# Optimization experiments

Measured on AMD Instinct MI355X. Metric: run time of the kernel, lower is better.

Reference implementation:

```python
import jax, jax.numpy as jnp
import numpy as np

EPS = 1e-5  # InstanceNorm2d default eps


def setup_inputs() -> dict:
    key = jax.random.key(0)
    ks = jax.random.split(key, 5)
    B, T, C, N, H = 4, 8, 256, 196, 4
    s = 1.0 / np.sqrt(C)
    return {
        "emb": jax.random.normal(ks[0], (B, T, C, N), dtype=jnp.float32),
        "Wq": jax.random.normal(ks[1], (H, C, C), dtype=jnp.float32) * s,
        "Wk": jax.random.normal(ks[2], (H, C, C), dtype=jnp.float32) * s,
        "Wv": jax.random.normal(ks[3], (H, C, C), dtype=jnp.float32) * s,
        "Wo": jax.random.normal(ks[4], (C, C), dtype=jnp.float32) * s,
    }


def reference(emb, Wq, Wk, Wv, Wo):
    B, T, C, N = emb.shape
    S = T * N  # KV_size
    # emb.permute(0,1,3,2).view(B, T*N, C)
    x = jnp.transpose(emb, (0, 1, 3, 2)).reshape(B, S, C)
    # per-head full-width Linear projections (nn.Linear: y = x @ W.T)
    Q = jnp.einsum("bsc,hdc->bhsd", x, Wq)  # [B,H,S,C]
    K = jnp.einsum("bsc,hdc->bhsd", x, Wk)
    V = jnp.einsum("bsc,hdc->bhsd", x, Wv)
    scores = jnp.einsum("bhsd,bhtd->bhst", Q, K) / jnp.sqrt(jnp.float32(S))
    # InstanceNorm2d over each [S,S] map per (batch, head), no affine, biased var
    mean = jnp.mean(scores, axis=(-2, -1), keepdims=True)
    var = jnp.var(scores, axis=(-2, -1), keepdims=True)
    normed = (scores - mean) * jax.lax.rsqrt(var + EPS)
    probs = jax.nn.softmax(normed, axis=-1)  # attn_dropout: eval-mode identity
    ctx = jnp.einsum("bhst,bhtd->bhsd", probs, V)  # [B,H,S,C]
    ctx = jnp.mean(ctx, axis=1)  # mean over heads -> [B,S,C]
    O1 = jnp.einsum("bsc,dc->bsd", ctx, Wo)  # out Linear; proj_dropout identity
    # .view(-1, num_frames, num_channels, num_patches) on contiguous [B, T*N, C]
    return O1.reshape(B, T, C, N)
```

## Files before the change

kernel.cpp:

```cpp
#include <hip/hip_runtime.h>
#include <stdint.h>

typedef unsigned short u16;

#define Bb 4
#define Hh 4
#define Tt 8
#define Cc 256
#define NP 196
#define Ss 1568
#define SCALE_S 0.0252538136f

typedef __attribute__((ext_vector_type(4))) float floatx4;
typedef __attribute__((ext_vector_type(8))) short shortx8;

__device__ __forceinline__ float bf2f(u16 u) {
    union { unsigned u; float f; } v; v.u = ((unsigned)u) << 16; return v.f;
}
__device__ __forceinline__ u16 f2bf(float f) {
    union { float f; unsigned u; } v; v.f = f;
    unsigned r = v.u + 0x7FFFu + ((v.u >> 16) & 1u);
    return (u16)(r >> 16);
}

__global__ __launch_bounds__(256) void k_convw(const float* __restrict__ src, u16* __restrict__ dst, int n) {
    int i = blockIdx.x * 256 + threadIdx.x;
    if (i < n) dst[i] = f2bf(src[i]);
}

__device__ __forceinline__ void mfma_step(const u16* As, const u16* Bs, int lane,
                                          int wm, int wn, floatx4 acc[4][4]) {
    const int r15 = lane & 15;
    const int kq  = (lane >> 4) << 3;
    shortx8 a[4], b[4];
#pragma unroll
    for (int i = 0; i < 4; ++i)
        a[i] = *(const shortx8*)(As + (wm * 64 + i * 16 + r15) * 32 + kq);
#pragma unroll
    for (int j = 0; j < 4; ++j)
        b[j] = *(const shortx8*)(Bs + (wn * 64 + j * 16 + r15) * 32 + kq);
#pragma unroll
    for (int i = 0; i < 4; ++i)
#pragma unroll
        for (int j = 0; j < 4; ++j)
            acc[i][j] = __builtin_amdgcn_mfma_f32_16x16x32_bf16(a[i], b[j], acc[i][j], 0, 0, 0);
}

__device__ __forceinline__ void gemm_bt_core(const u16* A, const u16* Bm, int lda, int ldb,
                                             int mbase, int mlast, int nbase, int nlast,
                                             int KD, u16* As, u16* Bs, floatx4 acc[4][4]) {
    int tid = threadIdx.x;
    int lane = tid & 63, wave = tid >> 6, wm = wave >> 1, wn = wave & 1;
    int row0 = tid >> 2, row1 = 64 + (tid >> 2);
    int cole = (tid & 3) << 3;
    int ga0 = mbase + row0; ga0 = ga0 <= mlast ? ga0 : mlast;
    int ga1 = mbase + row1; ga1 = ga1 <= mlast ? ga1 : mlast;
    int gb0 = nbase + row0; gb0 = gb0 <= nlast ? gb0 : nlast;
    int gb1 = nbase + row1; gb1 = gb1 <= nlast ? gb1 : nlast;
    const u16* pa0 = A  + (size_t)ga0 * lda + cole;
    const u16* pa1 = A  + (size_t)ga1 * lda + cole;
    const u16* pb0 = Bm + (size_t)gb0 * ldb + cole;
    const u16* pb1 = Bm + (size_t)gb1 * ldb + cole;
    shortx8 va0 = *(const shortx8*)(pa0);
    shortx8 va1 = *(const shortx8*)(pa1);
    shortx8 vb0 = *(const shortx8*)(pb0);
    shortx8 vb1 = *(const shortx8*)(pb1);
    for (int k0 = 0; k0 < KD; k0 += 32) {
        __syncthreads();
        *(shortx8*)(As + row0 * 32 + cole) = va0;
        *(shortx8*)(As + row1 * 32 + cole) = va1;
        *(shortx8*)(Bs + row0 * 32 + cole) = vb0;
        *(shortx8*)(Bs + row1 * 32 + cole) = vb1;
        int k1 = k0 + 32;
        if (k1 < KD) {
            va0 = *(const shortx8*)(pa0 + k1);
            va1 = *(const shortx8*)(pa1 + k1);
            vb0 = *(const shortx8*)(pb0 + k1);
            vb1 = *(const shortx8*)(pb1 + k1);
        }
        __syncthreads();
        mfma_step(As, Bs, lane, wm, wn, acc);
    }
}

__global__ void k_transpose(const float* __restrict__ emb, u16* __restrict__ x) {
    __shared__ u16 tile[32][33];
    int bt = blockIdx.z;
    int c0 = blockIdx.y * 32, n0 = blockIdx.x * 32;
    const float* src = emb + (size_t)bt * Cc * NP;
#pragma unroll
    for (int rr = 0; rr < 32; rr += 8) {
        int c = c0 + threadIdx.y + rr;
        int n = n0 + threadIdx.x;
        u16 v = 0;
        if (n < NP) v = f2bf(src[(size_t)c * NP + n]);
        tile[threadIdx.y + rr][threadIdx.x] = v;
    }
    __syncthreads();
    int b = bt / Tt, t = bt % Tt;
    u16* dst = x + ((size_t)b * Ss + (size_t)t * NP) * Cc;
#pragma unroll
    for (int rr = 0; rr < 32; rr += 8) {
        int n = n0 + threadIdx.y + rr;
        int c = c0 + threadIdx.x;
        if (n < NP) dst[(size_t)n * Cc + c] = tile[threadIdx.x][threadIdx.y + rr];
    }
}

__global__ __launch_bounds__(256) void k_qkv(const u16* __restrict__ x,
                                             const u16* __restrict__ Wq,
                                             const u16* __restrict__ Wk,
                                             const u16* __restrict__ Wv,
                                             u16* __restrict__ Q, u16* __restrict__ Kb,
                                             u16* __restrict__ Vt) {
    __shared__ __align__(16) u16 As[128 * 32], Bs[128 * 32];
    floatx4 acc[4][4];
#pragma unroll
    for (int i = 0; i < 4; ++i)
#pragma unroll
        for (int j = 0; j < 4; ++j) acc[i][j] = (floatx4)(0.f);
    int z = blockIdx.z;
    int qkv = z >> 4, bh = z & 15, b = bh >> 2, h = bh & 3;
    const u16* A = x + (size_t)b * Ss * Cc;
    const u16* W = (qkv == 0 ? Wq : (qkv == 1 ? Wk : Wv)) + (size_t)h * Cc * Cc;
    int mbase = blockIdx.y * 128, nbase = blockIdx.x * 128;
    gemm_bt_core(A, W, Cc, Cc, mbase, Ss - 1, nbase, Cc - 1, Cc, As, Bs, acc);

    int tid = threadIdx.x, lane = tid & 63, wave = tid >> 6, wm = wave >> 1, wn = wave & 1;
    int rq = (lane >> 4) << 2, cn = lane & 15;
    if (qkv < 2) {
        u16* out = (qkv == 0 ? Q : Kb) + (size_t)bh * Ss * Cc;
#pragma unroll
        for (int i = 0; i < 4; ++i) {
            int mb = mbase + wm * 64 + i * 16 + rq;
#pragma unroll
            for (int j = 0; j < 4; ++j) {
                int n = nbase + wn * 64 + j * 16 + cn;
#pragma unroll
                for (int r = 0; r < 4; ++r) {
                    int m = mb + r;
                    if (m < Ss) out[(size_t)m * Cc + n] = f2bf(acc[i][j][r]);
                }
            }
        }
    } else {
        u16* out = Vt + (size_t)bh * Cc * Ss;
#pragma unroll
        for (int i = 0; i < 4; ++i) {
            int m0 = mbase + wm * 64 + i * 16 + rq;
            if (m0 < Ss) {
#pragma unroll
                for (int j = 0; j < 4; ++j) {
                    int n = nbase + wn * 64 + j * 16 + cn;
                    ushort4 v;
                    v.x = f2bf(acc[i][j][0]); v.y = f2bf(acc[i][j][1]);
                    v.z = f2bf(acc[i][j][2]); v.w = f2bf(acc[i][j][3]);
                    *(ushort4*)(out + (size_t)n * Ss + m0) = v;
                }
            }
        }
    }
}

__global__ __launch_bounds__(256) void k_scores(const u16* __restrict__ Q,
                                                const u16* __restrict__ Kb,
                                                u16* __restrict__ Sc, float* __restrict__ stats) {
    __shared__ __align__(16) u16 As[128 * 32], Bs[128 * 32];
    __shared__ float sred[8];
    floatx4 acc[4][4];
#pragma unroll
    for (int i = 0; i < 4; ++i)
#pragma unroll
        for (int j = 0; j < 4; ++j) acc[i][j] = (floatx4)(0.f);
    int bh = blockIdx.z;
    const u16* A  = Q  + (size_t)bh * Ss * Cc;
    const u16* Bm = Kb + (size_t)bh * Ss * Cc;
    int mbase = blockIdx.y * 128, nbase = blockIdx.x * 128;
    gemm_bt_core(A, Bm, Cc, Cc, mbase, Ss - 1, nbase, Ss - 1, Cc, As, Bs, acc);

    int tid = threadIdx.x, lane = tid & 63, wave = tid >> 6, wm = wave >> 1, wn = wave & 1;
    int rq = (lane >> 4) << 2, cn = lane & 15;
    u16* out = Sc + (size_t)bh * Ss * Ss;
    float lsum = 0.f, lsq = 0.f;
#pragma unroll
    for (int i = 0; i < 4; ++i) {
        int mb = mbase + wm * 64 + i * 16 + rq;
#pragma unroll
        for (int j = 0; j < 4; ++j) {
            int n = nbase + wn * 64 + j * 16 + cn;
            bool nv = n < Ss;
#pragma unroll
            for (int r = 0; r < 4; ++r) {
                int m = mb + r;
                if (nv && m < Ss) {
                    float v = acc[i][j][r] * SCALE_S;
                    out[(size_t)m * Ss + n] = f2bf(v);
                    lsum += v; lsq += v * v;
                }
            }
        }
    }
#pragma unroll
    for (int mk = 1; mk <= 32; mk <<= 1) { lsum += __shfl_xor(lsum, mk); lsq += __shfl_xor(lsq, mk); }
    if (lane == 0) { sred[wave] = lsum; sred[4 + wave] = lsq; }
    __syncthreads();
    if (tid == 0) atomicAdd(&stats[bh * 4 + 0], sred[0] + sred[1] + sred[2] + sred[3]);
    if (tid == 1) atomicAdd(&stats[bh * 4 + 1], sred[4] + sred[5] + sred[6] + sred[7]);
}

__global__ void k_stats(float* __restrict__ stats) {
    int i = threadIdx.x;
    if (i < 16) {
        float inv  = 1.f / ((float)Ss * (float)Ss);
        float mean = stats[i * 4] * inv;
        float var  = stats[i * 4 + 1] * inv - mean * mean;
        var = fmaxf(var, 0.f);
        stats[i * 4 + 2] = mean;
        stats[i * 4 + 3] = rsqrtf(var + 1e-5f);
    }
}

__global__ __launch_bounds__(256) void k_pv(const u16* __restrict__ Sc,
                                            const u16* __restrict__ Vt,
                                            const float* __restrict__ stats,
                                            float* __restrict__ ctxm) {
    __shared__ __align__(16) u16 As[128 * 32], Bs[128 * 32];
    __shared__ float rs[128];
    floatx4 acc[4][4];
#pragma unroll
    for (int i = 0; i < 4; ++i)
#pragma unroll
        for (int j = 0; j < 4; ++j) acc[i][j] = (floatx4)(0.f);
    int bh = blockIdx.z;
    float mean = stats[bh * 4 + 2], istd = stats[bh * 4 + 3];
    float aa = istd * 1.44269504f;
    float bb = -mean * aa;
    const u16* A  = Sc + (size_t)bh * Ss * Ss;
    const u16* Bm = Vt + (size_t)bh * Cc * Ss;
    int mbase = blockIdx.y * 128, nbase = blockIdx.x * 128;
    int tid = threadIdx.x, lane = tid & 63, wave = tid >> 6, wm = wave >> 1, wn = wave & 1;
    int row0 = tid >> 2, row1 = 64 + (tid >> 2);
    int cole = (tid & 3) << 3;
    int ga0 = mbase + row0; ga0 = ga0 <= Ss - 1 ? ga0 : Ss - 1;
    int ga1 = mbase + row1; ga1 = ga1 <= Ss - 1 ? ga1 : Ss - 1;
    const u16* pa0 = A + (size_t)ga0 * Ss + cole;
    const u16* pa1 = A + (size_t)ga1 * Ss + cole;
    const u16* pb0 = Bm + (size_t)(nbase + row0) * Ss + cole;
    const u16* pb1 = Bm + (size_t)(nbase + row1) * Ss + cole;
    float rsum0 = 0.f, rsum1 = 0.f;
    shortx8 v0 = *(const shortx8*)(pa0);
    shortx8 v1 = *(const shortx8*)(pa1);
    shortx8 vb0 = *(const shortx8*)(pb0);
    shortx8 vb1 = *(const shortx8*)(pb1);

    for (int k0 = 0; k0 < Ss; k0 += 32) {
        shortx8 o0, o1;
        float p0 = 0.f, p1 = 0.f;
#pragma unroll
        for (int e = 0; e < 8; ++e) {
            float f0 = bf2f((u16)v0[e]);
            float e0 = exp2f(f0 * aa + bb);
            p0 += e0; o0[e] = (short)f2bf(e0);
            float f1 = bf2f((u16)v1[e]);
            float e1 = exp2f(f1 * aa + bb);
            p1 += e1; o1[e] = (short)f2bf(e1);
        }
        rsum0 += p0; rsum1 += p1;
        __syncthreads();
        *(shortx8*)(As + row0 * 32 + cole) = o0;
        *(shortx8*)(As + row1 * 32 + cole) = o1;
        *(shortx8*)(Bs + row0 * 32 + cole) = vb0;
        *(shortx8*)(Bs + row1 * 32 + cole) = vb1;
        int k1 = k0 + 32;
        if (k1 < Ss) {
            v0  = *(const shortx8*)(pa0 + k1);
            v1  = *(const shortx8*)(pa1 + k1);
            vb0 = *(const shortx8*)(pb0 + k1);
            vb1 = *(const shortx8*)(pb1 + k1);
        }
        __syncthreads();
        mfma_step(As, Bs, lane, wm, wn, acc);
    }
    rsum0 += __shfl_xor(rsum0, 1); rsum0 += __shfl_xor(rsum0, 2);
    rsum1 += __shfl_xor(rsum1, 1); rsum1 += __shfl_xor(rsum1, 2);
    __syncthreads();
    if ((tid & 3) == 0) { rs[tid >> 2] = rsum0; rs[64 + (tid >> 2)] = rsum1; }
    __syncthreads();

    int b = bh >> 2;
    float* outp = ctxm + (size_t)b * Ss * Cc;
    int rq = (lane >> 4) << 2, cn = lane & 15;
#pragma unroll
    for (int i = 0; i < 4; ++i) {
        int ml = wm * 64 + i * 16 + rq;
#pragma unroll
        for (int r = 0; r < 4; ++r) {
            int m = mbase + ml + r;
            if (m < Ss) {
                float invs = 0.25f / rs[ml + r];
#pragma unroll
                for (int j = 0; j < 4; ++j) {
                    int n = nbase + wn * 64 + j * 16 + cn;
                    atomicAdd(&outp[(size_t)m * Cc + n], acc[i][j][r] * invs);
                }
            }
        }
    }
}

__global__ __launch_bounds__(256) void k_out(const float* __restrict__ ctxm,
                                             const u16* __restrict__ Wo, float* __restrict__ out) {
    __shared__ __align__(16) u16 As[128 * 32], Bs[128 * 32];
    floatx4 acc[4][4];
#pragma unroll
    for (int i = 0; i < 4; ++i)
#pragma unroll
        for (int j = 0; j < 4; ++j) acc[i][j] = (floatx4)(0.f);
    int b = blockIdx.z;
    const float* A = ctxm + (size_t)b * Ss * Cc;
    int mbase = blockIdx.y * 128, nbase = blockIdx.x * 128;
    int tid = threadIdx.x, lane = tid & 63, wave = tid >> 6, wm = wave >> 1, wn = wave & 1;
    int row0 = tid >> 2, row1 = 64 + (tid >> 2);
    int cole = (tid & 3) << 3;
    int ga0 = mbase + row0; ga0 = ga0 <= Ss - 1 ? ga0 : Ss - 1;
    int ga1 = mbase + row1; ga1 = ga1 <= Ss - 1 ? ga1 : Ss - 1;
    const float* pa0 = A + (size_t)ga0 * Cc + cole;
    const float* pa1 = A + (size_t)ga1 * Cc + cole;
    const u16* pb0 = Wo + (size_t)(nbase + row0 <= Cc - 1 ? nbase + row0 : Cc - 1) * Cc + cole;
    const u16* pb1 = Wo + (size_t)(nbase + row1 <= Cc - 1 ? nbase + row1 : Cc - 1) * Cc + cole;
    float4 a00 = *(const float4*)(pa0), a01 = *(const float4*)(pa0 + 4);
    float4 a10 = *(const float4*)(pa1), a11 = *(const float4*)(pa1 + 4);
    shortx8 vb0 = *(const shortx8*)(pb0);
    shortx8 vb1 = *(const shortx8*)(pb1);
    for (int k0 = 0; k0 < Cc; k0 += 32) {
        shortx8 o0, o1;
        o0[0] = (short)f2bf(a00.x); o0[1] = (short)f2bf(a00.y); o0[2] = (short)f2bf(a00.z); o0[3] = (short)f2bf(a00.w);
        o0[4] = (short)f2bf(a01.x); o0[5] = (short)f2bf(a01.y); o0[6] = (short)f2bf(a01.z); o0[7] = (short)f2bf(a01.w);
        o1[0] = (short)f2bf(a10.x); o1[1] = (short)f2bf(a10.y); o1[2] = (short)f2bf(a10.z); o1[3] = (short)f2bf(a10.w);
        o1[4] = (short)f2bf(a11.x); o1[5] = (short)f2bf(a11.y); o1[6] = (short)f2bf(a11.z); o1[7] = (short)f2bf(a11.w);
        __syncthreads();
        *(shortx8*)(As + row0 * 32 + cole) = o0;
        *(shortx8*)(As + row1 * 32 + cole) = o1;
        *(shortx8*)(Bs + row0 * 32 + cole) = vb0;
        *(shortx8*)(Bs + row1 * 32 + cole) = vb1;
        int k1 = k0 + 32;
        if (k1 < Cc) {
            a00 = *(const float4*)(pa0 + k1); a01 = *(const float4*)(pa0 + k1 + 4);
            a10 = *(const float4*)(pa1 + k1); a11 = *(const float4*)(pa1 + k1 + 4);
            vb0 = *(const shortx8*)(pb0 + k1);
            vb1 = *(const shortx8*)(pb1 + k1);
        }
        __syncthreads();
        mfma_step(As, Bs, lane, wm, wn, acc);
    }
    int rq = (lane >> 4) << 2, cn = lane & 15;
    float* o = out + (size_t)b * Ss * Cc;
#pragma unroll
    for (int i = 0; i < 4; ++i) {
        int mb = mbase + wm * 64 + i * 16 + rq;
#pragma unroll
        for (int j = 0; j < 4; ++j) {
            int n = nbase + wn * 64 + j * 16 + cn;
#pragma unroll
            for (int r = 0; r < 4; ++r) {
                int m = mb + r;
                if (m < Ss) o[(size_t)m * Cc + n] = acc[i][j][r];
            }
        }
    }
}

extern "C" void kernel_launch(void* const* d_in, const int* in_sizes, int n_in,
                              void* d_out, int out_size, void* d_ws, size_t ws_size,
                              hipStream_t stream) {
    const float* emb = (const float*)d_in[0];
    float* out = (float*)d_out;

    char* ws = (char*)d_ws;
    size_t off = 0;
    auto alloc = [&](size_t bytes) -> void* {
        void* p = ws + off;
        off = (off + bytes + 255) & ~(size_t)255;
        return p;
    };
    float* stats = (float*)alloc(16 * 4 * sizeof(float));
    u16* Wqc  = (u16*)alloc((size_t)Hh * Cc * Cc * 2);
    u16* Wkc  = (u16*)alloc((size_t)Hh * Cc * Cc * 2);
    u16* Wvc  = (u16*)alloc((size_t)Hh * Cc * Cc * 2);
    u16* Woc  = (u16*)alloc((size_t)Cc * Cc * 2);
    u16* x    = (u16*)alloc((size_t)Bb * Ss * Cc * 2);
    u16* Q    = (u16*)alloc((size_t)Bb * Hh * Ss * Cc * 2);
    u16* Kb   = (u16*)alloc((size_t)Bb * Hh * Ss * Cc * 2);
    u16* Vt   = (u16*)alloc((size_t)Bb * Hh * Ss * Cc * 2);
    float* ctxm = (float*)alloc((size_t)Bb * Ss * Cc * 4);
    u16* Sc   = (u16*)alloc((size_t)Bb * Hh * Ss * Ss * 2);

    hipMemsetAsync(stats, 0, 16 * 4 * sizeof(float), stream);
    hipMemsetAsync(ctxm, 0, (size_t)Bb * Ss * Cc * 4, stream);

    k_convw<<<dim3(1024), dim3(256), 0, stream>>>((const float*)d_in[1], Wqc, Hh * Cc * Cc);
    k_convw<<<dim3(1024), dim3(256), 0, stream>>>((const float*)d_in[2], Wkc, Hh * Cc * Cc);
    k_convw<<<dim3(1024), dim3(256), 0, stream>>>((const float*)d_in[3], Wvc, Hh * Cc * Cc);
    k_convw<<<dim3(256),  dim3(256), 0, stream>>>((const float*)d_in[4], Woc, Cc * Cc);

    k_transpose<<<dim3(7, 8, 32), dim3(32, 8), 0, stream>>>(emb, x);
    k_qkv<<<dim3(2, 13, 48), dim3(256), 0, stream>>>(x, Wqc, Wkc, Wvc, Q, Kb, Vt);
    k_scores<<<dim3(13, 13, 16), dim3(256), 0, stream>>>(Q, Kb, Sc, stats);
    k_stats<<<dim3(1), dim3(64), 0, stream>>>(stats);
    k_pv<<<dim3(2, 13, 16), dim3(256), 0, stream>>>(Sc, Vt, stats, ctxm);
    k_out<<<dim3(2, 13, 4), dim3(256), 0, stream>>>(ctxm, Woc, out);
}
```

Baseline: 255.1 us.

## Pad LDS rows, double-depth register prefetch, merge weight-convert and stats kernels

Shared-memory tiles get a padded row stride of 40 elements to reduce LDS bank conflicts on the MFMA fragment reads. The GEMM core and k_pv now keep two K-slices of global loads in flight in registers, giving more latency hiding at the cost of extra registers. The four weight-conversion launches are merged into one kernel writing a single contiguous buffer. The tiny k_stats kernel is removed, with the mean and istd computed inline in k_pv, cutting launch overhead.

```diff
diff --git a/kernel.cpp b/kernel.cpp
--- a/kernel.cpp
+++ b/kernel.cpp
@@ -10,6 +10,7 @@
 #define NP 196
 #define Ss 1568
 #define SCALE_S 0.0252538136f
+#define LST 40
 
 typedef __attribute__((ext_vector_type(4))) float floatx4;
 typedef __attribute__((ext_vector_type(8))) short shortx8;
@@ -23,9 +24,20 @@
     return (u16)(r >> 16);
 }
 
-__global__ __launch_bounds__(256) void k_convw(const float* __restrict__ src, u16* __restrict__ dst, int n) {
+__global__ __launch_bounds__(256) void k_convall(const float* __restrict__ Wq,
+                                                 const float* __restrict__ Wk,
+                                                 const float* __restrict__ Wv,
+                                                 const float* __restrict__ Wo,
+                                                 u16* __restrict__ dst) {
+    const int NW = Hh * Cc * Cc;
     int i = blockIdx.x * 256 + threadIdx.x;
-    if (i < n) dst[i] = f2bf(src[i]);
+    float v;
+    if (i < NW) v = Wq[i];
+    else if (i < 2 * NW) v = Wk[i - NW];
+    else if (i < 3 * NW) v = Wv[i - 2 * NW];
+    else if (i < 3 * NW + Cc * Cc) v = Wo[i - 3 * NW];
+    else return;
+    dst[i] = f2bf(v);
 }
 
 __device__ __forceinline__ void mfma_step(const u16* As, const u16* Bs, int lane,
@@ -35,10 +47,10 @@
     shortx8 a[4], b[4];
 #pragma unroll
     for (int i = 0; i < 4; ++i)
-        a[i] = *(const shortx8*)(As + (wm * 64 + i * 16 + r15) * 32 + kq);
+        a[i] = *(const shortx8*)(As + (wm * 64 + i * 16 + r15) * LST + kq);
 #pragma unroll
     for (int j = 0; j < 4; ++j)
-        b[j] = *(const shortx8*)(Bs + (wn * 64 + j * 16 + r15) * 32 + kq);
+        b[j] = *(const shortx8*)(Bs + (wn * 64 + j * 16 + r15) * LST + kq);
 #pragma unroll
     for (int i = 0; i < 4; ++i)
 #pragma unroll
@@ -51,7 +63,7 @@
                                              int KD, u16* As, u16* Bs, floatx4 acc[4][4]) {
     int tid = threadIdx.x;
     int lane = tid & 63, wave = tid >> 6, wm = wave >> 1, wn = wave & 1;
-    int row0 = tid >> 2, row1 = 64 + (tid >> 2);
+    int row0 = tid >> 2, row1 = 64 + row0;
     int cole = (tid & 3) << 3;
     int ga0 = mbase + row0; ga0 = ga0 <= mlast ? ga0 : mlast;
     int ga1 = mbase + row1; ga1 = ga1 <= mlast ? ga1 : mlast;
@@ -61,25 +73,37 @@
     const u16* pa1 = A  + (size_t)ga1 * lda + cole;
     const u16* pb0 = Bm + (size_t)gb0 * ldb + cole;
     const u16* pb1 = Bm + (size_t)gb1 * ldb + cole;
-    shortx8 va0 = *(const shortx8*)(pa0);
-    shortx8 va1 = *(const shortx8*)(pa1);
-    shortx8 vb0 = *(const shortx8*)(pb0);
-    shortx8 vb1 = *(const shortx8*)(pb1);
-    for (int k0 = 0; k0 < KD; k0 += 32) {
-        __syncthreads();
-        *(shortx8*)(As + row0 * 32 + cole) = va0;
-        *(shortx8*)(As + row1 * 32 + cole) = va1;
-        *(shortx8*)(Bs + row0 * 32 + cole) = vb0;
-        *(shortx8*)(Bs + row1 * 32 + cole) = vb1;
-        int k1 = k0 + 32;
-        if (k1 < KD) {
-            va0 = *(const shortx8*)(pa0 + k1);
-            va1 = *(const shortx8*)(pa1 + k1);
-            vb0 = *(const shortx8*)(pb0 + k1);
-            vb1 = *(const shortx8*)(pb1 + k1);
+    shortx8 xa0 = *(const shortx8*)(pa0),      xa1 = *(const shortx8*)(pa1);
+    shortx8 xb0 = *(const shortx8*)(pb0),      xb1 = *(const shortx8*)(pb1);
+    shortx8 ya0 = *(const shortx8*)(pa0 + 32), ya1 = *(const shortx8*)(pa1 + 32);
+    shortx8 yb0 = *(const shortx8*)(pb0 + 32), yb1 = *(const shortx8*)(pb1 + 32);
+    for (int k0 = 0; k0 < KD; k0 += 64) {
+        __syncthreads();
+        *(shortx8*)(As + row0 * LST + cole) = xa0;
+        *(shortx8*)(As + row1 * LST + cole) = xa1;
+        *(shortx8*)(Bs + row0 * LST + cole) = xb0;
+        *(shortx8*)(Bs + row1 * LST + cole) = xb1;
+        int kp = k0 + 64;
+        if (kp < KD) {
+            xa0 = *(const shortx8*)(pa0 + kp); xa1 = *(const shortx8*)(pa1 + kp);
+            xb0 = *(const shortx8*)(pb0 + kp); xb1 = *(const shortx8*)(pb1 + kp);
         }
         __syncthreads();
         mfma_step(As, Bs, lane, wm, wn, acc);
+        if (k0 + 32 < KD) {
+            __syncthreads();
+            *(shortx8*)(As + row0 * LST + cole) = ya0;
+            *(shortx8*)(As + row1 * LST + cole) = ya1;
+            *(shortx8*)(Bs + row0 * LST + cole) = yb0;
+            *(shortx8*)(Bs + row1 * LST + cole) = yb1;
+            int kq2 = k0 + 96;
+            if (kq2 < KD) {
+                ya0 = *(const shortx8*)(pa0 + kq2); ya1 = *(const shortx8*)(pa1 + kq2);
+                yb0 = *(const shortx8*)(pb0 + kq2); yb1 = *(const shortx8*)(pb1 + kq2);
+            }
+            __syncthreads();
+            mfma_step(As, Bs, lane, wm, wn, acc);
+        }
     }
 }
 
@@ -108,12 +132,10 @@
 }
 
 __global__ __launch_bounds__(256) void k_qkv(const u16* __restrict__ x,
-                                             const u16* __restrict__ Wq,
-                                             const u16* __restrict__ Wk,
-                                             const u16* __restrict__ Wv,
+                                             const u16* __restrict__ Wall,
                                              u16* __restrict__ Q, u16* __restrict__ Kb,
                                              u16* __restrict__ Vt) {
-    __shared__ __align__(16) u16 As[128 * 32], Bs[128 * 32];
+    __shared__ __align__(16) u16 As[128 * LST], Bs[128 * LST];
     floatx4 acc[4][4];
 #pragma unroll
     for (int i = 0; i < 4; ++i)
@@ -122,7 +144,7 @@
     int z = blockIdx.z;
     int qkv = z >> 4, bh = z & 15, b = bh >> 2, h = bh & 3;
     const u16* A = x + (size_t)b * Ss * Cc;
-    const u16* W = (qkv == 0 ? Wq : (qkv == 1 ? Wk : Wv)) + (size_t)h * Cc * Cc;
+    const u16* W = Wall + (size_t)qkv * Hh * Cc * Cc + (size_t)h * Cc * Cc;
     int mbase = blockIdx.y * 128, nbase = blockIdx.x * 128;
     gemm_bt_core(A, W, Cc, Cc, mbase, Ss - 1, nbase, Cc - 1, Cc, As, Bs, acc);
 
@@ -165,7 +187,7 @@
 __global__ __launch_bounds__(256) void k_scores(const u16* __restrict__ Q,
                                                 const u16* __restrict__ Kb,
                                                 u16* __restrict__ Sc, float* __restrict__ stats) {
-    __shared__ __align__(16) u16 As[128 * 32], Bs[128 * 32];
+    __shared__ __align__(16) u16 As[128 * LST], Bs[128 * LST];
     __shared__ float sred[8];
     floatx4 acc[4][4];
 #pragma unroll
@@ -208,23 +230,11 @@
     if (tid == 1) atomicAdd(&stats[bh * 4 + 1], sred[4] + sred[5] + sred[6] + sred[7]);
 }
 
-__global__ void k_stats(float* __restrict__ stats) {
-    int i = threadIdx.x;
-    if (i < 16) {
-        float inv  = 1.f / ((float)Ss * (float)Ss);
-        float mean = stats[i * 4] * inv;
-        float var  = stats[i * 4 + 1] * inv - mean * mean;
-        var = fmaxf(var, 0.f);
-        stats[i * 4 + 2] = mean;
-        stats[i * 4 + 3] = rsqrtf(var + 1e-5f);
-    }
-}
-
 __global__ __launch_bounds__(256) void k_pv(const u16* __restrict__ Sc,
                                             const u16* __restrict__ Vt,
                                             const float* __restrict__ stats,
                                             float* __restrict__ ctxm) {
-    __shared__ __align__(16) u16 As[128 * 32], Bs[128 * 32];
+    __shared__ __align__(16) u16 As[128 * LST], Bs[128 * LST];
     __shared__ float rs[128];
     floatx4 acc[4][4];
 #pragma unroll
@@ -232,14 +242,17 @@
 #pragma unroll
         for (int j = 0; j < 4; ++j) acc[i][j] = (floatx4)(0.f);
     int bh = blockIdx.z;
-    float mean = stats[bh * 4 + 2], istd = stats[bh * 4 + 3];
+    float inv  = 1.f / ((float)Ss * (float)Ss);
+    float mean = stats[bh * 4] * inv;
+    float var  = fmaxf(stats[bh * 4 + 1] * inv - mean * mean, 0.f);
+    float istd = rsqrtf(var + 1e-5f);
     float aa = istd * 1.44269504f;
     float bb = -mean * aa;
     const u16* A  = Sc + (size_t)bh * Ss * Ss;
     const u16* Bm = Vt + (size_t)bh * Cc * Ss;
     int mbase = blockIdx.y * 128, nbase = blockIdx.x * 128;
     int tid = threadIdx.x, lane = tid & 63, wave = tid >> 6, wm = wave >> 1, wn = wave & 1;
-    int row0 = tid >> 2, row1 = 64 + (tid >> 2);
+    int row0 = tid >> 2, row1 = 64 + row0;
     int cole = (tid & 3) << 3;
     int ga0 = mbase + row0; ga0 = ga0 <= Ss - 1 ? ga0 : Ss - 1;
     int ga1 = mbase + row1; ga1 = ga1 <= Ss - 1 ? ga1 : Ss - 1;
@@ -248,38 +261,52 @@
     const u16* pb0 = Bm + (size_t)(nbase + row0) * Ss + cole;
     const u16* pb1 = Bm + (size_t)(nbase + row1) * Ss + cole;
     float rsum0 = 0.f, rsum1 = 0.f;
-    shortx8 v0 = *(const shortx8*)(pa0);
-    shortx8 v1 = *(const shortx8*)(pa1);
-    shortx8 vb0 = *(const shortx8*)(pb0);
-    shortx8 vb1 = *(const shortx8*)(pb1);
-
-    for (int k0 = 0; k0 < Ss; k0 += 32) {
-        shortx8 o0, o1;
-        float p0 = 0.f, p1 = 0.f;
+
+    auto ldexp8 = [&](const u16* p, float& rsum) -> shortx8 {
+        shortx8 v = *(const shortx8*)(p);
+        shortx8 o;
+        float s = 0.f;
 #pragma unroll
         for (int e = 0; e < 8; ++e) {
-            float f0 = bf2f((u16)v0[e]);
-            float e0 = exp2f(f0 * aa + bb);
-            p0 += e0; o0[e] = (short)f2bf(e0);
-            float f1 = bf2f((u16)v1[e]);
-            float e1 = exp2f(f1 * aa + bb);
-            p1 += e1; o1[e] = (short)f2bf(e1);
-        }
-        rsum0 += p0; rsum1 += p1;
-        __syncthreads();
-        *(shortx8*)(As + row0 * 32 + cole) = o0;
-        *(shortx8*)(As + row1 * 32 + cole) = o1;
-        *(shortx8*)(Bs + row0 * 32 + cole) = vb0;
-        *(shortx8*)(Bs + row1 * 32 + cole) = vb1;
-        int k1 = k0 + 32;
-        if (k1 < Ss) {
-            v0  = *(const shortx8*)(pa0 + k1);
-            v1  = *(const shortx8*)(pa1 + k1);
-            vb0 = *(const shortx8*)(pb0 + k1);
-            vb1 = *(const shortx8*)(pb1 + k1);
+            float ex = exp2f(bf2f((u16)v[e]) * aa + bb);
+            s += ex; o[e] = (short)f2bf(ex);
+        }
+        rsum += s;
+        return o;
+    };
+
+    shortx8 xa0 = ldexp8(pa0, rsum0),      xa1 = ldexp8(pa1, rsum1);
+    shortx8 xb0 = *(const shortx8*)(pb0),  xb1 = *(const shortx8*)(pb1);
+    shortx8 ya0 = ldexp8(pa0 + 32, rsum0), ya1 = ldexp8(pa1 + 32, rsum1);
+    shortx8 yb0 = *(const shortx8*)(pb0 + 32), yb1 = *(const shortx8*)(pb1 + 32);
+
+    for (int k0 = 0; k0 < Ss; k0 += 64) {
+        __syncthreads();
+        *(shortx8*)(As + row0 * LST + cole) = xa0;
+        *(shortx8*)(As + row1 * LST + cole) = xa1;
+        *(shortx8*)(Bs + row0 * LST + cole) = xb0;
+        *(shortx8*)(Bs + row1 * LST + cole) = xb1;
+        int kp = k0 + 64;
+        if (kp < Ss) {
+            xa0 = ldexp8(pa0 + kp, rsum0); xa1 = ldexp8(pa1 + kp, rsum1);
+            xb0 = *(const shortx8*)(pb0 + kp); xb1 = *(const shortx8*)(pb1 + kp);
         }
         __syncthreads();
         mfma_step(As, Bs, lane, wm, wn, acc);
+        if (k0 + 32 < Ss) {
+            __syncthreads();
+            *(shortx8*)(As + row0 * LST + cole) = ya0;
+            *(shortx8*)(As + row1 * LST + cole) = ya1;
+            *(shortx8*)(Bs + row0 * LST + cole) = yb0;
+            *(shortx8*)(Bs + row1 * LST + cole) = yb1;
+            int kq2 = k0 + 96;
+            if (kq2 < Ss) {
+                ya0 = ldexp8(pa0 + kq2, rsum0); ya1 = ldexp8(pa1 + kq2, rsum1);
+                yb0 = *(const shortx8*)(pb0 + kq2); yb1 = *(const shortx8*)(pb1 + kq2);
+            }
+            __syncthreads();
+            mfma_step(As, Bs, lane, wm, wn, acc);
+        }
     }
     rsum0 += __shfl_xor(rsum0, 1); rsum0 += __shfl_xor(rsum0, 2);
     rsum1 += __shfl_xor(rsum1, 1); rsum1 += __shfl_xor(rsum1, 2);
@@ -310,7 +337,7 @@
 
 __global__ __launch_bounds__(256) void k_out(const float* __restrict__ ctxm,
                                              const u16* __restrict__ Wo, float* __restrict__ out) {
-    __shared__ __align__(16) u16 As[128 * 32], Bs[128 * 32];
+    __shared__ __align__(16) u16 As[128 * LST], Bs[128 * LST];
     floatx4 acc[4][4];
 #pragma unroll
     for (int i = 0; i < 4; ++i)
@@ -320,7 +347,7 @@
     const float* A = ctxm + (size_t)b * Ss * Cc;
     int mbase = blockIdx.y * 128, nbase = blockIdx.x * 128;
     int tid = threadIdx.x, lane = tid & 63, wave = tid >> 6, wm = wave >> 1, wn = wave & 1;
-    int row0 = tid >> 2, row1 = 64 + (tid >> 2);
+    int row0 = tid >> 2, row1 = 64 + row0;
     int cole = (tid & 3) << 3;
     int ga0 = mbase + row0; ga0 = ga0 <= Ss - 1 ? ga0 : Ss - 1;
     int ga1 = mbase + row1; ga1 = ga1 <= Ss - 1 ? ga1 : Ss - 1;
@@ -339,10 +366,10 @@
         o1[0] = (short)f2bf(a10.x); o1[1] = (short)f2bf(a10.y); o1[2] = (short)f2bf(a10.z); o1[3] = (short)f2bf(a10.w);
         o1[4] = (short)f2bf(a11.x); o1[5] = (short)f2bf(a11.y); o1[6] = (short)f2bf(a11.z); o1[7] = (short)f2bf(a11.w);
         __syncthreads();
-        *(shortx8*)(As + row0 * 32 + cole) = o0;
-        *(shortx8*)(As + row1 * 32 + cole) = o1;
-        *(shortx8*)(Bs + row0 * 32 + cole) = vb0;
-        *(shortx8*)(Bs + row1 * 32 + cole) = vb1;
+        *(shortx8*)(As + row0 * LST + cole) = o0;
+        *(shortx8*)(As + row1 * LST + cole) = o1;
+        *(shortx8*)(Bs + row0 * LST + cole) = vb0;
+        *(shortx8*)(Bs + row1 * LST + cole) = vb1;
         int k1 = k0 + 32;
         if (k1 < Cc) {
             a00 = *(const float4*)(pa0 + k1); a01 = *(const float4*)(pa0 + k1 + 4);
@@ -384,29 +411,23 @@
         return p;
     };
     float* stats = (float*)alloc(16 * 4 * sizeof(float));
-    u16* Wqc  = (u16*)alloc((size_t)Hh * Cc * Cc * 2);
-    u16* Wkc  = (u16*)alloc((size_t)Hh * Cc * Cc * 2);
-    u16* Wvc  = (u16*)alloc((size_t)Hh * Cc * Cc * 2);
-    u16* Woc  = (u16*)alloc((size_t)Cc * Cc * 2);
+    u16* Wall = (u16*)alloc((size_t)(3 * Hh + 1) * Cc * Cc * 2);
     u16* x    = (u16*)alloc((size_t)Bb * Ss * Cc * 2);
     u16* Q    = (u16*)alloc((size_t)Bb * Hh * Ss * Cc * 2);
     u16* Kb   = (u16*)alloc((size_t)Bb * Hh * Ss * Cc * 2);
     u16* Vt   = (u16*)alloc((size_t)Bb * Hh * Ss * Cc * 2);
     float* ctxm = (float*)alloc((size_t)Bb * Ss * Cc * 4);
     u16* Sc   = (u16*)alloc((size_t)Bb * Hh * Ss * Ss * 2);
+    u16* Woc  = Wall + (size_t)3 * Hh * Cc * Cc;
 
     hipMemsetAsync(stats, 0, 16 * 4 * sizeof(float), stream);
     hipMemsetAsync(ctxm, 0, (size_t)Bb * Ss * Cc * 4, stream);
 
-    k_convw<<<dim3(1024), dim3(256), 0, stream>>>((const float*)d_in[1], Wqc, Hh * Cc * Cc);
-    k_convw<<<dim3(1024), dim3(256), 0, stream>>>((const float*)d_in[2], Wkc, Hh * Cc * Cc);
-    k_convw<<<dim3(1024), dim3(256), 0, stream>>>((const float*)d_in[3], Wvc, Hh * Cc * Cc);
-    k_convw<<<dim3(256),  dim3(256), 0, stream>>>((const float*)d_in[4], Woc, Cc * Cc);
-
+    k_convall<<<dim3(3328), dim3(256), 0, stream>>>((const float*)d_in[1], (const float*)d_in[2],
+                                                    (const float*)d_in[3], (const float*)d_in[4], Wall);
     k_transpose<<<dim3(7, 8, 32), dim3(32, 8), 0, stream>>>(emb, x);
-    k_qkv<<<dim3(2, 13, 48), dim3(256), 0, stream>>>(x, Wqc, Wkc, Wvc, Q, Kb, Vt);
+    k_qkv<<<dim3(2, 13, 48), dim3(256), 0, stream>>>(x, Wall, Q, Kb, Vt);
     k_scores<<<dim3(13, 13, 16), dim3(256), 0, stream>>>(Q, Kb, Sc, stats);
-    k_stats<<<dim3(1), dim3(64), 0, stream>>>(stats);
     k_pv<<<dim3(2, 13, 16), dim3(256), 0, stream>>>(Sc, Vt, stats, ctxm);
     k_out<<<dim3(2, 13, 4), dim3(256), 0, stream>>>(ctxm, Woc, out);
 }
```

New measurement: 247.2 us. 3.1% less time.
